# Optimization experiments

Hardware: AMD Instinct MI355X
Metric: run time of the kernel (lower is better)

The kernel has to match this reference:

```python
import jax, jax.numpy as jnp
import numpy as np

N = 50000        # num nodes
E = 800000       # num edges
R = 2            # num relations
HID = 256        # hid_dim
Q = HID // 4     # per-feature-block projection size
NC = 2           # num classes
DES, TW, NP_, CP = 768, 768, 5, 3


def setup_inputs():
    key = jax.random.key(0)
    ks = jax.random.split(key, 32)
    w = lambda i, shape: jax.random.normal(ks[i], shape, dtype=jnp.float32) * 0.05
    z = lambda d: jnp.zeros((d,), jnp.float32)
    return {
        'des': jax.random.normal(ks[0], (N, DES), jnp.float32),
        'tweet': jax.random.normal(ks[1], (N, TW), jnp.float32),
        'num_prop': jax.random.normal(ks[2], (N, NP_), jnp.float32),
        'cat_prop': jax.random.normal(ks[3], (N, CP), jnp.float32),
        'edge_index': jax.random.randint(ks[4], (2, E), 0, N),
        'edge_type': jax.random.randint(ks[5], (E,), 0, R),
        'w_des': w(6, (DES, Q)), 'b_des': z(Q),
        'w_tweet': w(7, (TW, Q)), 'b_tweet': z(Q),
        'w_num': w(8, (NP_, Q)), 'b_num': z(Q),
        'w_cat': w(9, (CP, Q)), 'b_cat': z(Q),
        'w_in': w(10, (HID, HID)), 'b_in': z(HID),
        'weight1': w(11, (R, HID, HID)), 'root1': w(12, (HID, HID)), 'bias1': z(HID),
        'weight2': w(13, (R, HID, HID)), 'root2': w(14, (HID, HID)), 'bias2': z(HID),
        'w_out': w(15, (HID, NC)), 'b_out': z(NC),
    }


def _rgcn_layer(x, weight, root, bias, src, dst, edge_type):
    # T stage: per-relation transform + root transform, bias, relu.
    h_rel = jax.nn.relu(jnp.einsum('nh,rho->rno', x, weight) + bias)   # [R,N,H]
    h_root = jax.nn.relu(x @ root + bias)                              # [N,H]
    # P stage: gather per-relation messages, mean-aggregate at dst, sum over relations.
    msg = h_rel[edge_type, src]                                        # [E,H] gather
    seg = edge_type * N + dst                                          # relation-disjoint segments
    sums = jax.ops.segment_sum(msg, seg, num_segments=R * N).reshape(R, N, -1)
    cnt = jax.ops.segment_sum(jnp.ones((msg.shape[0],), msg.dtype), seg,
                              num_segments=R * N).reshape(R, N, 1)
    mean = sums / jnp.maximum(cnt, 1.0)                                # per-relation mean aggr
    return mean.sum(0) + h_root


def _lrelu(x):
    return jax.nn.leaky_relu(x, 0.01)


def reference(des, tweet, num_prop, cat_prop, edge_index, edge_type,
              w_des, b_des, w_tweet, b_tweet, w_num, b_num, w_cat, b_cat,
              w_in, b_in, weight1, root1, bias1, weight2, root2, bias2,
              w_out, b_out):
    src, dst = edge_index[0], edge_index[1]
    d = _lrelu(des @ w_des + b_des)
    t = _lrelu(tweet @ w_tweet + b_tweet)
    n = _lrelu(num_prop @ w_num + b_num)
    c = _lrelu(cat_prop @ w_cat + b_cat)
    x = jnp.concatenate([d, t, n, c], axis=1)          # [N, HID]
    x = _lrelu(x @ w_in + b_in)
    x = _rgcn_layer(x, weight1, root1, bias1, src, dst, edge_type)
    x = _rgcn_layer(x, weight2, root2, bias2, src, dst, edge_type)
    return x @ w_out + b_out                           # [N, NC] logits (MLP last=True)
```

## Files before the change

kernel.cpp:

```cpp
#include <hip/hip_runtime.h>

#define NN 50000
#define EE 800000
#define HD 256
#define NSEG (2 * NN)
#define CHUNK 2048
#define NB ((NSEG + CHUNK - 1) / CHUNK)

typedef unsigned short u16;
typedef unsigned long long u64;
typedef short bf16x8 __attribute__((ext_vector_type(8)));
typedef float f32x4 __attribute__((ext_vector_type(4)));

__device__ __forceinline__ u16 f2bf_rne(float f) {
    unsigned u = __float_as_uint(f);
    return (u16)((u + 0x7FFF + ((u >> 16) & 1)) >> 16);
}
__device__ __forceinline__ void split_tr(float v, u16& h, u16& l) {
    unsigned u = __float_as_uint(v);
    h = (u16)(u >> 16);
    l = f2bf_rne(v - __uint_as_float(u & 0xFFFF0000u));
}

__device__ __forceinline__ int xcd_swizzle(int orig, int nwg) {
    int q = nwg >> 3, r = nwg & 7;
    int xcd = orig & 7, idx = orig >> 3;
    return (xcd < r ? xcd * (q + 1) : r * (q + 1) + (xcd - r) * q) + idx;
}

__device__ __forceinline__ void g2l16(const void* g, void* l) {
    __builtin_amdgcn_global_load_lds(
        (const __attribute__((address_space(1))) void*)g,
        (__attribute__((address_space(3))) void*)l, 16, 0, 0);
}

__device__ __forceinline__ int swz2(int row) { return (row & 2) | ((row >> 2) & 1); }

__device__ __forceinline__ void stage_bf16(const u16* __restrict__ G, u16* S,
                                           int base_rc, int maxrc, int K, int k0, int tid) {
#pragma unroll
    for (int s = 0; s < 2; s++) {
        int slot = tid + s * 256;
        int row = slot >> 2, gg = slot & 3;
        int gsrc = gg ^ swz2(row);
        int arow = base_rc + row; arow = arow < maxrc ? arow : maxrc - 1;
        g2l16(G + (size_t)arow * K + k0 + gsrc * 8, S + ((tid & ~63) + s * 256) * 8);
    }
}

template<int MODE>
__global__ __launch_bounds__(256) void gemm_bf16s(
    const u16* __restrict__ Ag, const u16* __restrict__ Bg,
    const float* __restrict__ bias,
    u16* __restrict__ O1, float* __restrict__ O2,
    int M, int nxb)
{
    __shared__ __align__(16) u16 sA[2][128 * 32];
    __shared__ __align__(16) u16 sB[2][128 * 32];
    const int wgid = xcd_swizzle(blockIdx.x, gridDim.x);
    const int brow = (wgid / nxb) * 128, bcol = (wgid % nxb) * 128;
    const int tid = threadIdx.x, lane = tid & 63, w = tid >> 6;
    const int wr = w >> 1, wc = w & 1;
    const int r15 = lane & 15, g = lane >> 4;
    const int fsw = (g ^ swz2(r15)) * 8;

    f32x4 acc[4][4];
#pragma unroll
    for (int mi = 0; mi < 4; mi++)
#pragma unroll
        for (int ni = 0; ni < 4; ni++) acc[mi][ni] = (f32x4){0.f, 0.f, 0.f, 0.f};

    auto stage_step = [&](int k0, int b) {
        stage_bf16(Ag, sA[b], brow, M, 256, k0, tid);
        stage_bf16(Bg, sB[b], bcol, 1 << 30, 256, k0, tid);
    };
    auto compute_step = [&](int b) {
        bf16x8 af[4], bf[4];
#pragma unroll
        for (int mi = 0; mi < 4; mi++) {
            int idx = (wr * 64 + mi * 16 + r15) * 32 + fsw;
            af[mi] = *(const bf16x8*)&sA[b][idx];
        }
#pragma unroll
        for (int ni = 0; ni < 4; ni++) {
            int idx = (wc * 64 + ni * 16 + r15) * 32 + fsw;
            bf[ni] = *(const bf16x8*)&sB[b][idx];
        }
#pragma unroll
        for (int mi = 0; mi < 4; mi++)
#pragma unroll
            for (int ni = 0; ni < 4; ni++)
                acc[mi][ni] = __builtin_amdgcn_mfma_f32_16x16x32_bf16(af[mi], bf[ni], acc[mi][ni], 0, 0, 0);
    };

    stage_step(0, 0);
    stage_step(32, 1);
#pragma unroll
    for (int t = 0; t < 7; t++) {
        asm volatile("s_waitcnt vmcnt(4)" ::: "memory");
        __builtin_amdgcn_s_barrier();
        compute_step(t & 1);
        __builtin_amdgcn_s_barrier();
        if (t + 2 < 8) stage_step((t + 2) * 32, t & 1);
    }
    asm volatile("s_waitcnt vmcnt(0)" ::: "memory");
    __builtin_amdgcn_s_barrier();
    compute_step(1);

#pragma unroll
    for (int mi = 0; mi < 4; mi++) {
#pragma unroll
        for (int ni = 0; ni < 4; ni++) {
            int col = bcol + wc * 64 + ni * 16 + r15;
            float bsv = bias[col & (HD - 1)];
            int rbase = brow + wr * 64 + mi * 16 + g * 4;
#pragma unroll
            for (int r = 0; r < 4; r++) {
                int grow = rbase + r;
                if (grow >= M) continue;
                float v = acc[mi][ni][r] + bsv;
                if (MODE == 1) {
                    v = v > 0.f ? v : 0.01f * v;
                    O1[(size_t)grow * HD + col] = f2bf_rne(v);
                } else {
                    v = fmaxf(v, 0.f);
                    if (col < 2 * HD) {
                        O1[((size_t)(col >> 8) * NN + grow) * HD + (col & (HD - 1))] = f2bf_rne(v);
                    } else {
                        O2[(size_t)grow * HD + (col & (HD - 1))] = v;
                    }
                }
            }
        }
    }
}

__global__ __launch_bounds__(128) void gemm_projW(
    const float* __restrict__ A0, const float* __restrict__ A1,
    const u16* __restrict__ B0, const u16* __restrict__ B1,
    const float* __restrict__ bias0, const float* __restrict__ bias1,
    u16* __restrict__ Ch)
{
    __shared__ __align__(16) u16 lds[2 * 2 * 2 * 640];
    const int p = blockIdx.x & 1;
    const float* __restrict__ A = p ? A1 : A0;
    const u16* __restrict__ Bp = p ? B1 : B0;
    const float* __restrict__ bias = p ? bias1 : bias0;
    const int coff = p * 64;
    const int lane = threadIdx.x & 63, w = threadIdx.x >> 6;
    const int wrow = (blockIdx.x >> 1) * 32 + w * 16;
    const int r15 = lane & 15, g = lane >> 4;
    const int lbase = w * 2560;

    size_t aoff[2];
#pragma unroll
    for (int i = 0; i < 2; i++) {
        int row = wrow + (lane >> 3) + 8 * i;
        row = row < NN ? row : NN - 1;
        aoff[i] = (size_t)row * 768 + (lane & 7) * 4;
    }
    size_t boff[4];
#pragma unroll
    for (int ni = 0; ni < 4; ni++)
        boff[ni] = (size_t)(ni * 64 + lane) * 8;

    f32x4 acc[4];
#pragma unroll
    for (int ni = 0; ni < 4; ni++) acc[ni] = (f32x4){0.f, 0.f, 0.f, 0.f};

    float4 Ar0[2], Ar1[2];
    uint4 Bs0[4], Bs1[4];

    auto loadA = [&](int t, float4 (&d)[2]) {
#pragma unroll
        for (int i = 0; i < 2; i++) d[i] = *(const float4*)&A[aoff[i] + t * 32];
    };
    auto loadB = [&](int t, uint4 (&d)[4]) {
#pragma unroll
        for (int ni = 0; ni < 4; ni++) d[ni] = *(const uint4*)&Bp[boff[ni] + (size_t)t * 2048];
    };
    auto writeA = [&](const float4 (&s)[2], int buf) {
#pragma unroll
        for (int i = 0; i < 2; i++) {
            int row2 = (lane >> 3) + 8 * i;
            unsigned e0 = __float_as_uint(s[i].x), e1 = __float_as_uint(s[i].y),
                     e2 = __float_as_uint(s[i].z), e3 = __float_as_uint(s[i].w);
            unsigned h0 = __builtin_amdgcn_perm(e1, e0, 0x07060302u);
            unsigned h1 = __builtin_amdgcn_perm(e3, e2, 0x07060302u);
            unsigned q0 = __float_as_uint(s[i].x - __uint_as_float(e0 & 0xFFFF0000u));
            unsigned q1 = __float_as_uint(s[i].y - __uint_as_float(e1 & 0xFFFF0000u));
            unsigned q2 = __float_as_uint(s[i].z - __uint_as_float(e2 & 0xFFFF0000u));
            unsigned q3 = __float_as_uint(s[i].w - __uint_as_float(e3 & 0xFFFF0000u));
            unsigned l0 = __builtin_amdgcn_perm(q1, q0, 0x07060302u);
            unsigned l1 = __builtin_amdgcn_perm(q3, q2, 0x07060302u);
            int idx = lbase + buf * 1280 + row2 * 40 + (lane & 7) * 4;
            *(u64*)&lds[idx] = (u64)h0 | ((u64)h1 << 32);
            *(u64*)&lds[idx + 640] = (u64)l0 | ((u64)l1 << 32);
        }
    };
    auto compute = [&](int buf, const uint4 (&Bv)[4]) {
        bf16x8 afh, afl;
        {
            int idx = lbase + buf * 1280 + r15 * 40 + g * 8;
            afh = *(const bf16x8*)&lds[idx];
            afl = *(const bf16x8*)&lds[idx + 640];
        }
#pragma unroll
        for (int ni = 0; ni < 4; ni++) {
            bf16x8 bb = __builtin_bit_cast(bf16x8, Bv[ni]);
            acc[ni] = __builtin_amdgcn_mfma_f32_16x16x32_bf16(afh, bb, acc[ni], 0, 0, 0);
            acc[ni] = __builtin_amdgcn_mfma_f32_16x16x32_bf16(afl, bb, acc[ni], 0, 0, 0);
        }
    };

    loadA(0, Ar0); loadB(0, Bs0);
    writeA(Ar0, 0);
    loadA(1, Ar1); loadB(1, Bs1);
    for (int tt = 0; tt < 11; ++tt) {
        int t0 = 2 * tt;
        loadA(t0 + 2, Ar0);
        compute(0, Bs0);
        loadB(t0 + 2, Bs0);
        writeA(Ar1, 1);
        loadA(t0 + 3, Ar1);
        compute(1, Bs1);
        loadB(t0 + 3, Bs1);
        writeA(Ar0, 0);
    }
    compute(0, Bs0);
    writeA(Ar1, 1);
    compute(1, Bs1);

    u16* tlh = &lds[lbase];
#pragma unroll
    for (int ni = 0; ni < 4; ni++) {
        int col = ni * 16 + r15;
        float bsv = bias[col];
#pragma unroll
        for (int r = 0; r < 4; r++) {
            int row = g * 4 + r;
            float v = acc[ni][r] + bsv;
            v = v > 0.f ? v : 0.01f * v;
            tlh[row * 72 + col] = f2bf_rne(v);
        }
    }
    asm volatile("s_waitcnt lgkmcnt(0)" ::: "memory");
    __builtin_amdgcn_sched_barrier(0);
    {
        int row = lane >> 2, cb = (lane & 3) * 16;
        int grow = wrow + row;
        if (grow < NN) {
#pragma unroll
            for (int j = 0; j < 2; j++) {
                uint4 hv = *(const uint4*)&tlh[row * 72 + cb + j * 8];
                *(uint4*)&Ch[(size_t)grow * HD + coff + cb + j * 8] = hv;
            }
        }
    }
}

__global__ void conv_all(
    const float* __restrict__ w_des, const float* __restrict__ w_tw,
    const float* __restrict__ w_in,
    const float* __restrict__ weight1, const float* __restrict__ root1,
    const float* __restrict__ weight2, const float* __restrict__ root2,
    u16* __restrict__ desB, u16* __restrict__ twB,
    u16* __restrict__ winB, u16* __restrict__ cat1, u16* __restrict__ cat2)
{
    const int HSZ = HD * HD;
    int idx = blockIdx.x * 256 + threadIdx.x;
    if (idx < 98304) {
        const float* W = idx < 49152 ? w_des : w_tw;
        u16* Bf = idx < 49152 ? desB : twB;
        int i = idx < 49152 ? idx : idx - 49152;
        int k = i >> 6, n = i & 63;
        int t = k >> 5, kk = k & 31, g = kk >> 3, j = kk & 7;
        int lane = g * 16 + (n & 15), ni = n >> 4;
        Bf[(size_t)((t * 4 + ni) * 64 + lane) * 8 + j] = f2bf_rne(W[i]);
        return;
    }
    int jdx = idx - 98304;
    int seg = jdx >> 16;
    if (seg >= 7) return;
    int i = jdx & 65535;
    const float* srcs[7] = {w_in, weight1, weight1 + HSZ, root1,
                            weight2, weight2 + HSZ, root2};
    u16* dsts[7] = {winB, cat1, cat1 + 256 * 256, cat1 + 512 * 256,
                    cat2, cat2 + 256 * 256, cat2 + 512 * 256};
    int k = i >> 8, n = i & 255;
    dsts[seg][(size_t)n * 256 + k] = f2bf_rne(srcs[seg][i]);
}

__global__ __launch_bounds__(256) void gemm_f32s2(
    const float* __restrict__ A0, const float* __restrict__ A1,
    const float* __restrict__ B0, const float* __restrict__ B1,
    const float* __restrict__ bias0, const float* __restrict__ bias1,
    u16* __restrict__ Ch)
{
    const int p = blockIdx.x;
    const float* __restrict__ A = p ? A1 : A0;
    const float* __restrict__ B = p ? B1 : B0;
    const float* __restrict__ bias = p ? bias1 : bias0;
    const int lda = p ? 3 : 5, K = lda, coff = p ? 192 : 128;

    __shared__ float As[8][64 + 4];
    __shared__ float Bs[8][64 + 4];
    const int tid = threadIdx.x;
    const int tx = tid % 16, ty = tid / 16;
    const int brow = blockIdx.y * 64;
    float acc[4][4];
#pragma unroll
    for (int i = 0; i < 4; i++)
#pragma unroll
        for (int j = 0; j < 4; j++) acc[i][j] = 0.f;

#pragma unroll 2
    for (int idx = tid; idx < 64 * 8; idx += 256) {
        int m = idx / 8, k = idx % 8;
        int gr = brow + m;
        As[k][m] = (gr < NN && k < K) ? A[(size_t)gr * lda + k] : 0.f;
    }
#pragma unroll 2
    for (int idx = tid; idx < 8 * 64; idx += 256) {
        int k = idx / 64, n = idx % 64;
        Bs[k][n] = (k < K) ? B[(size_t)k * 64 + n] : 0.f;
    }
    __syncthreads();
#pragma unroll
    for (int k = 0; k < 8; k++) {
        float a[4], b[4];
#pragma unroll
        for (int i = 0; i < 4; i++) a[i] = As[k][ty * 4 + i];
#pragma unroll
        for (int j = 0; j < 4; j++) b[j] = Bs[k][tx * 4 + j];
#pragma unroll
        for (int i = 0; i < 4; i++)
#pragma unroll
            for (int j = 0; j < 4; j++) acc[i][j] = fmaf(a[i], b[j], acc[i][j]);
    }

#pragma unroll
    for (int i = 0; i < 4; i++) {
        int gr = brow + ty * 4 + i;
        if (gr >= NN) continue;
#pragma unroll
        for (int j = 0; j < 4; j++) {
            int gc = tx * 4 + j;
            float v = acc[i][j] + bias[gc];
            v = v > 0.f ? v : 0.01f * v;
            Ch[(size_t)gr * HD + coff + gc] = f2bf_rne(v);
        }
    }
}

__global__ void count_seg(const int* __restrict__ ei, const int* __restrict__ et,
                          int* __restrict__ segc)
{
    int e = blockIdx.x * blockDim.x + threadIdx.x;
    if (e < EE) {
        int dst = ei[EE + e];
        int r = et[e];
        atomicAdd(&segc[r * NN + dst], 1);
    }
}

__global__ __launch_bounds__(256) void scan_local(const int* __restrict__ segc,
                                                  int* __restrict__ offs,
                                                  int* __restrict__ bsum)
{
    int b = blockIdx.x;
    int base = b * CHUNK;
    int tid = threadIdx.x;
    int lane = tid & 63, wave = tid >> 6;
    __shared__ int wsum[4];
    int vals[8];
    int i0 = base + tid * 8;
    int s = 0;
    if (i0 + 7 < NSEG) {
        int4 v0 = *(const int4*)&segc[i0];
        int4 v1 = *(const int4*)&segc[i0 + 4];
        vals[0] = v0.x; vals[1] = v0.y; vals[2] = v0.z; vals[3] = v0.w;
        vals[4] = v1.x; vals[5] = v1.y; vals[6] = v1.z; vals[7] = v1.w;
    } else {
#pragma unroll
        for (int j = 0; j < 8; j++) vals[j] = (i0 + j < NSEG) ? segc[i0 + j] : 0;
    }
#pragma unroll
    for (int j = 0; j < 8; j++) s += vals[j];
    int v = s;
#pragma unroll
    for (int off = 1; off < 64; off <<= 1) {
        int u = __shfl_up(v, off);
        if (lane >= off) v += u;
    }
    if (lane == 63) wsum[wave] = v;
    __syncthreads();
    int wbase = 0;
#pragma unroll
    for (int ww = 0; ww < 4; ww++) if (ww < wave) wbase += wsum[ww];
    int run = wbase + v - s;
#pragma unroll
    for (int j = 0; j < 8; j++) {
        run += vals[j];
        int i = i0 + j;
        if (i < NSEG) offs[i + 1] = run;
    }
    if (tid == 0) {
        int t = 0;
#pragma unroll
        for (int ww = 0; ww < 4; ww++) t += wsum[ww];
        bsum[b] = t;
    }
}

__global__ void scan_bsum(const int* __restrict__ bsum, int* __restrict__ bbase)
{
    int lane = threadIdx.x;
    int c = (lane < NB) ? bsum[lane] : 0;
    int v = c;
#pragma unroll
    for (int off = 1; off < 64; off <<= 1) {
        int u = __shfl_up(v, off);
        if (lane >= off) v += u;
    }
    if (lane < NB) bbase[lane] = v - c;
}

__global__ void add_base(int* __restrict__ offs, const int* __restrict__ bbase)
{
    int i = blockIdx.x * blockDim.x + threadIdx.x;
    if (i < NSEG) offs[i + 1] += bbase[i / CHUNK];
    if (i == 0) offs[0] = 0;
}

__global__ void fill_src(const int* __restrict__ ei, const int* __restrict__ et,
                         const int* __restrict__ offs, int* __restrict__ cursor,
                         int* __restrict__ src_list)
{
    int e = blockIdx.x * blockDim.x + threadIdx.x;
    if (e < EE) {
        int src = ei[e];
        int dst = ei[EE + e];
        int s = et[e] * NN + dst;
        int pos = offs[s] + atomicAdd(&cursor[s], 1);
        src_list[pos] = src;
    }
}

template<int OUTM>
__global__ __launch_bounds__(256) void gather_mean_b(
    const u16* __restrict__ hrelb,
    const int* __restrict__ offs,
    const int* __restrict__ src_list,
    const float* __restrict__ basein,
    u16* __restrict__ Oh,
    const float* __restrict__ wout, const float* __restrict__ bout,
    float* __restrict__ logits)
{
    int d = blockIdx.x * 4 + (threadIdx.x >> 6);
    if (d >= NN) return;
    int lane = threadIdx.x & 63;
    f32x4 acc = {0.f, 0.f, 0.f, 0.f};
#pragma unroll
    for (int r = 0; r < 2; r++) {
        int s = r * NN + d;
        int start = offs[s], end = offs[s + 1];
        if (start == end) continue;
        f32x4 a = {0.f, 0.f, 0.f, 0.f};
        const u16* hb = hrelb + (size_t)r * NN * HD;
        for (int i = start; i < end; i++) {
            int src = src_list[i];
            uint2 wv = *(const uint2*)(hb + (size_t)src * HD + lane * 4);
            a.x += __uint_as_float(wv.x << 16);
            a.y += __uint_as_float(wv.x & 0xFFFF0000u);
            a.z += __uint_as_float(wv.y << 16);
            a.w += __uint_as_float(wv.y & 0xFFFF0000u);
        }
        float inv = 1.0f / (float)(end - start);
        acc.x += a.x * inv; acc.y += a.y * inv;
        acc.z += a.z * inv; acc.w += a.w * inv;
    }
    float4 b = ((const float4*)(basein + (size_t)d * HD))[lane];
    float v0 = b.x + acc.x, v1 = b.y + acc.y, v2 = b.z + acc.z, v3 = b.w + acc.w;
    if (OUTM == 0) {
        uint2 uh;
        uh.x = (unsigned)f2bf_rne(v0) | ((unsigned)f2bf_rne(v1) << 16);
        uh.y = (unsigned)f2bf_rne(v2) | ((unsigned)f2bf_rne(v3) << 16);
        *(uint2*)(Oh + (size_t)d * HD + lane * 4) = uh;
    } else {
        int k = lane * 4;
        float a0 = v0 * wout[(k + 0) * 2 + 0] + v1 * wout[(k + 1) * 2 + 0]
                 + v2 * wout[(k + 2) * 2 + 0] + v3 * wout[(k + 3) * 2 + 0];
        float a1 = v0 * wout[(k + 0) * 2 + 1] + v1 * wout[(k + 1) * 2 + 1]
                 + v2 * wout[(k + 2) * 2 + 1] + v3 * wout[(k + 3) * 2 + 1];
#pragma unroll
        for (int off = 32; off > 0; off >>= 1) {
            a0 += __shfl_down(a0, off);
            a1 += __shfl_down(a1, off);
        }
        if (lane == 0) {
            logits[(size_t)d * 2 + 0] = a0 + bout[0];
            logits[(size_t)d * 2 + 1] = a1 + bout[1];
        }
    }
}

extern "C" void kernel_launch(void* const* d_in, const int* in_sizes, int n_in,
                              void* d_out, int out_size, void* d_ws, size_t ws_size,
                              hipStream_t stream)
{
    const float* des   = (const float*)d_in[0];
    const float* tweet = (const float*)d_in[1];
    const float* nump  = (const float*)d_in[2];
    const float* catp  = (const float*)d_in[3];
    const int*   ei    = (const int*)d_in[4];
    const int*   et    = (const int*)d_in[5];
    const float* w_des = (const float*)d_in[6],  *b_des = (const float*)d_in[7];
    const float* w_tw  = (const float*)d_in[8],  *b_tw  = (const float*)d_in[9];
    const float* w_num = (const float*)d_in[10], *b_num = (const float*)d_in[11];
    const float* w_cat = (const float*)d_in[12], *b_cat = (const float*)d_in[13];
    const float* w_in  = (const float*)d_in[14], *b_in  = (const float*)d_in[15];
    const float* weight1 = (const float*)d_in[16], *root1 = (const float*)d_in[17], *bias1 = (const float*)d_in[18];
    const float* weight2 = (const float*)d_in[19], *root2 = (const float*)d_in[20], *bias2 = (const float*)d_in[21];
    const float* w_out = (const float*)d_in[22], *b_out = (const float*)d_in[23];
    float* outp = (float*)d_out;

    const int HSZ = HD * HD, PSZ = 768 * 64;

    float* base  = (float*)d_ws;
    u16*   hrelb = (u16*)(base + (size_t)NN * HD);
    u16*   xh    = hrelb + (size_t)2 * NN * HD;
    u16*   yh    = xh + (size_t)NN * HD;
    int*   offs  = (int*)(yh + (size_t)NN * HD);
    int*   segc  = offs + (NSEG + 1);
    int*   srcl  = segc + NSEG;
    int*   bsum  = srcl + EE;
    int*   bbase = bsum + NB;
    uintptr_t wp = ((uintptr_t)(bbase + NB) + 15) & ~(uintptr_t)15;
    u16* desB = (u16*)wp;
    u16* twB  = desB + PSZ;
    u16* winB = twB + PSZ;
    u16* cat1 = winB + HSZ;
    u16* cat2 = cat1 + 3 * HSZ;

    hipMemsetAsync(segc, 0, NSEG * sizeof(int), stream);
    count_seg<<<(EE + 255) / 256, 256, 0, stream>>>(ei, et, segc);
    scan_local<<<NB, 256, 0, stream>>>(segc, offs, bsum);
    scan_bsum<<<1, 64, 0, stream>>>(bsum, bbase);
    add_base<<<(NSEG + 255) / 256, 256, 0, stream>>>(offs, bbase);
    hipMemsetAsync(segc, 0, NSEG * sizeof(int), stream);
    fill_src<<<(EE + 255) / 256, 256, 0, stream>>>(ei, et, offs, segc, srcl);

    const int CONV_TOT = 98304 + 7 * 65536;
    conv_all<<<(CONV_TOT + 255) / 256, 256, 0, stream>>>(
        w_des, w_tw, w_in, weight1, root1, weight2, root2,
        desB, twB, winB, cat1, cat2);

    const int NYB = (NN + 127) / 128;
    const int NWB = (NN + 31) / 32;

    gemm_projW<<<2 * NWB, 128, 0, stream>>>(des, tweet, desB, twB, b_des, b_tw, xh);
    dim3 gsm(2, (NN + 63) / 64);
    gemm_f32s2<<<gsm, 256, 0, stream>>>(nump, catp, w_num, w_cat, b_num, b_cat, xh);

    gemm_bf16s<1><<<2 * NYB, 256, 0, stream>>>(xh, winB, b_in, yh, nullptr, NN, 2);

    gemm_bf16s<2><<<6 * NYB, 256, 0, stream>>>(yh, cat1, bias1, hrelb, base, NN, 6);
    gather_mean_b<0><<<(NN + 3) / 4, 256, 0, stream>>>(hrelb, offs, srcl, base, xh, nullptr, nullptr, nullptr);

    gemm_bf16s<2><<<6 * NYB, 256, 0, stream>>>(xh, cat2, bias2, hrelb, base, NN, 6);
    gather_mean_b<1><<<(NN + 3) / 4, 256, 0, stream>>>(hrelb, offs, srcl, base, nullptr, w_out, b_out, outp);
}
```

Before: 529.6 us.

## Merge independent prologue kernels into heterogeneous mega-launches to cut launch gaps

Independent kernels are combined into heterogeneous launches that branch on block index. The des/tweet projection, small num/cat projection, edge counting and weight conversion now share one launch, and the w_in GEMM shares another with the CSR fill. The fill reuses the count array as a decrementing cursor via atomicSub, which removes the second memset. This is meant to cut launch overhead and let the independent stages overlap on the GPU, at the cost of uneven block shapes within one launch and LDS sized for the largest branch.

```diff
diff --git a/kernel.cpp b/kernel.cpp
--- a/kernel.cpp
+++ b/kernel.cpp
@@ -16,11 +16,6 @@
     unsigned u = __float_as_uint(f);
     return (u16)((u + 0x7FFF + ((u >> 16) & 1)) >> 16);
 }
-__device__ __forceinline__ void split_tr(float v, u16& h, u16& l) {
-    unsigned u = __float_as_uint(v);
-    h = (u16)(u >> 16);
-    l = f2bf_rne(v - __uint_as_float(u & 0xFFFF0000u));
-}
 
 __device__ __forceinline__ int xcd_swizzle(int orig, int nwg) {
     int q = nwg >> 3, r = nwg & 7;
@@ -49,15 +44,15 @@
 }
 
 template<int MODE>
-__global__ __launch_bounds__(256) void gemm_bf16s(
+__device__ __forceinline__ void gemm_body(
+    u16* __restrict__ sA, u16* __restrict__ sB,
+    int bid, int nwg,
     const u16* __restrict__ Ag, const u16* __restrict__ Bg,
     const float* __restrict__ bias,
     u16* __restrict__ O1, float* __restrict__ O2,
     int M, int nxb)
 {
-    __shared__ __align__(16) u16 sA[2][128 * 32];
-    __shared__ __align__(16) u16 sB[2][128 * 32];
-    const int wgid = xcd_swizzle(blockIdx.x, gridDim.x);
+    const int wgid = xcd_swizzle(bid, nwg);
     const int brow = (wgid / nxb) * 128, bcol = (wgid % nxb) * 128;
     const int tid = threadIdx.x, lane = tid & 63, w = tid >> 6;
     const int wr = w >> 1, wc = w & 1;
@@ -71,20 +66,20 @@
         for (int ni = 0; ni < 4; ni++) acc[mi][ni] = (f32x4){0.f, 0.f, 0.f, 0.f};
 
     auto stage_step = [&](int k0, int b) {
-        stage_bf16(Ag, sA[b], brow, M, 256, k0, tid);
-        stage_bf16(Bg, sB[b], bcol, 1 << 30, 256, k0, tid);
+        stage_bf16(Ag, sA + b * 4096, brow, M, 256, k0, tid);
+        stage_bf16(Bg, sB + b * 4096, bcol, 1 << 30, 256, k0, tid);
     };
     auto compute_step = [&](int b) {
         bf16x8 af[4], bf[4];
 #pragma unroll
         for (int mi = 0; mi < 4; mi++) {
             int idx = (wr * 64 + mi * 16 + r15) * 32 + fsw;
-            af[mi] = *(const bf16x8*)&sA[b][idx];
+            af[mi] = *(const bf16x8*)&sA[b * 4096 + idx];
         }
 #pragma unroll
         for (int ni = 0; ni < 4; ni++) {
             int idx = (wc * 64 + ni * 16 + r15) * 32 + fsw;
-            bf[ni] = *(const bf16x8*)&sB[b][idx];
+            bf[ni] = *(const bf16x8*)&sB[b * 4096 + idx];
         }
 #pragma unroll
         for (int mi = 0; mi < 4; mi++)
@@ -135,20 +130,32 @@
     }
 }
 
-__global__ __launch_bounds__(128) void gemm_projW(
+template<int MODE>
+__global__ __launch_bounds__(256) void gemm_bf16s(
+    const u16* __restrict__ Ag, const u16* __restrict__ Bg,
+    const float* __restrict__ bias,
+    u16* __restrict__ O1, float* __restrict__ O2,
+    int M, int nxb)
+{
+    __shared__ __align__(16) u16 sA[2 * 4096];
+    __shared__ __align__(16) u16 sB[2 * 4096];
+    gemm_body<MODE>(sA, sB, blockIdx.x, gridDim.x, Ag, Bg, bias, O1, O2, M, nxb);
+}
+
+__device__ __forceinline__ void projW_body(
+    u16* __restrict__ lds, int bid,
     const float* __restrict__ A0, const float* __restrict__ A1,
     const u16* __restrict__ B0, const u16* __restrict__ B1,
     const float* __restrict__ bias0, const float* __restrict__ bias1,
     u16* __restrict__ Ch)
 {
-    __shared__ __align__(16) u16 lds[2 * 2 * 2 * 640];
-    const int p = blockIdx.x & 1;
+    const int p = bid & 1;
     const float* __restrict__ A = p ? A1 : A0;
     const u16* __restrict__ Bp = p ? B1 : B0;
     const float* __restrict__ bias = p ? bias1 : bias0;
     const int coff = p * 64;
     const int lane = threadIdx.x & 63, w = threadIdx.x >> 6;
-    const int wrow = (blockIdx.x >> 1) * 32 + w * 16;
+    const int wrow = (bid >> 1) * 32 + w * 16;
     const int r15 = lane & 15, g = lane >> 4;
     const int lbase = w * 2560;
 
@@ -259,86 +266,57 @@
     }
 }
 
-__global__ void conv_all(
-    const float* __restrict__ w_des, const float* __restrict__ w_tw,
-    const float* __restrict__ w_in,
-    const float* __restrict__ weight1, const float* __restrict__ root1,
-    const float* __restrict__ weight2, const float* __restrict__ root2,
-    u16* __restrict__ desB, u16* __restrict__ twB,
-    u16* __restrict__ winB, u16* __restrict__ cat1, u16* __restrict__ cat2)
-{
-    const int HSZ = HD * HD;
-    int idx = blockIdx.x * 256 + threadIdx.x;
-    if (idx < 98304) {
-        const float* W = idx < 49152 ? w_des : w_tw;
-        u16* Bf = idx < 49152 ? desB : twB;
-        int i = idx < 49152 ? idx : idx - 49152;
-        int k = i >> 6, n = i & 63;
-        int t = k >> 5, kk = k & 31, g = kk >> 3, j = kk & 7;
-        int lane = g * 16 + (n & 15), ni = n >> 4;
-        Bf[(size_t)((t * 4 + ni) * 64 + lane) * 8 + j] = f2bf_rne(W[i]);
-        return;
-    }
-    int jdx = idx - 98304;
-    int seg = jdx >> 16;
-    if (seg >= 7) return;
-    int i = jdx & 65535;
-    const float* srcs[7] = {w_in, weight1, weight1 + HSZ, root1,
-                            weight2, weight2 + HSZ, root2};
-    u16* dsts[7] = {winB, cat1, cat1 + 256 * 256, cat1 + 512 * 256,
-                    cat2, cat2 + 256 * 256, cat2 + 512 * 256};
-    int k = i >> 8, n = i & 255;
-    dsts[seg][(size_t)n * 256 + k] = f2bf_rne(srcs[seg][i]);
-}
-
-__global__ __launch_bounds__(256) void gemm_f32s2(
-    const float* __restrict__ A0, const float* __restrict__ A1,
-    const float* __restrict__ B0, const float* __restrict__ B1,
-    const float* __restrict__ bias0, const float* __restrict__ bias1,
+__device__ __forceinline__ void smallproj_body(
+    float* __restrict__ smem, int sbid,
+    const float* __restrict__ nump, const float* __restrict__ catp,
+    const float* __restrict__ w_num, const float* __restrict__ w_cat,
+    const float* __restrict__ b_num, const float* __restrict__ b_cat,
     u16* __restrict__ Ch)
 {
-    const int p = blockIdx.x;
-    const float* __restrict__ A = p ? A1 : A0;
-    const float* __restrict__ B = p ? B1 : B0;
-    const float* __restrict__ bias = p ? bias1 : bias0;
-    const int lda = p ? 3 : 5, K = lda, coff = p ? 192 : 128;
-
-    __shared__ float As[8][64 + 4];
-    __shared__ float Bs[8][64 + 4];
+    const int NSB = (NN + 31) / 32;
+    const int p = sbid >= NSB;
+    const int brow = (p ? sbid - NSB : sbid) * 32;
+    const float* __restrict__ A = p ? catp : nump;
+    const float* __restrict__ B = p ? w_cat : w_num;
+    const float* __restrict__ bias = p ? b_cat : b_num;
+    const int K = p ? 3 : 5, coff = p ? 192 : 128;
     const int tid = threadIdx.x;
-    const int tx = tid % 16, ty = tid / 16;
-    const int brow = blockIdx.y * 64;
+    float* As = smem;
+    float* Bs = smem + 8 * 36;
+
+#pragma unroll
+    for (int s = 0; s < 2; s++) {
+        int idx = tid + s * 128;
+        int m = idx >> 3, k = idx & 7;
+        int gr = brow + m;
+        As[k * 36 + m] = (gr < NN && k < K) ? A[(size_t)gr * K + k] : 0.f;
+    }
+#pragma unroll
+    for (int s = 0; s < 4; s++) {
+        int idx = tid + s * 128;
+        int k = idx >> 6, n = idx & 63;
+        Bs[k * 68 + n] = (k < K) ? B[k * 64 + n] : 0.f;
+    }
+    __syncthreads();
+
+    const int tx = tid & 15, ty = tid >> 4;
     float acc[4][4];
 #pragma unroll
     for (int i = 0; i < 4; i++)
 #pragma unroll
         for (int j = 0; j < 4; j++) acc[i][j] = 0.f;
-
-#pragma unroll 2
-    for (int idx = tid; idx < 64 * 8; idx += 256) {
-        int m = idx / 8, k = idx % 8;
-        int gr = brow + m;
-        As[k][m] = (gr < NN && k < K) ? A[(size_t)gr * lda + k] : 0.f;
-    }
-#pragma unroll 2
-    for (int idx = tid; idx < 8 * 64; idx += 256) {
-        int k = idx / 64, n = idx % 64;
-        Bs[k][n] = (k < K) ? B[(size_t)k * 64 + n] : 0.f;
-    }
-    __syncthreads();
 #pragma unroll
     for (int k = 0; k < 8; k++) {
         float a[4], b[4];
 #pragma unroll
-        for (int i = 0; i < 4; i++) a[i] = As[k][ty * 4 + i];
-#pragma unroll
-        for (int j = 0; j < 4; j++) b[j] = Bs[k][tx * 4 + j];
+        for (int i = 0; i < 4; i++) a[i] = As[k * 36 + ty * 4 + i];
+#pragma unroll
+        for (int j = 0; j < 4; j++) b[j] = Bs[k * 68 + tx * 4 + j];
 #pragma unroll
         for (int i = 0; i < 4; i++)
 #pragma unroll
             for (int j = 0; j < 4; j++) acc[i][j] = fmaf(a[i], b[j], acc[i][j]);
     }
-
 #pragma unroll
     for (int i = 0; i < 4; i++) {
         int gr = brow + ty * 4 + i;
@@ -353,15 +331,95 @@
     }
 }
 
-__global__ void count_seg(const int* __restrict__ ei, const int* __restrict__ et,
-                          int* __restrict__ segc)
-{
-    int e = blockIdx.x * blockDim.x + threadIdx.x;
+__global__ __launch_bounds__(128) void mega1(
+    const float* __restrict__ des, const float* __restrict__ tweet,
+    const u16* __restrict__ desB, const u16* __restrict__ twB,
+    const float* __restrict__ b_des, const float* __restrict__ b_tw,
+    u16* __restrict__ xh,
+    const float* __restrict__ nump, const float* __restrict__ catp,
+    const float* __restrict__ w_num, const float* __restrict__ w_cat,
+    const float* __restrict__ b_num, const float* __restrict__ b_cat,
+    const int* __restrict__ ei, const int* __restrict__ et, int* __restrict__ segc,
+    const float* __restrict__ w_in,
+    const float* __restrict__ weight1, const float* __restrict__ root1,
+    const float* __restrict__ weight2, const float* __restrict__ root2,
+    u16* __restrict__ winB, u16* __restrict__ cat1, u16* __restrict__ cat2,
+    int nproj, int nsmall, int ncount)
+{
+    __shared__ __align__(16) u16 smem[5120];
+    int bid = blockIdx.x;
+    if (bid < nproj) {
+        projW_body(smem, bid, des, tweet, desB, twB, b_des, b_tw, xh);
+        return;
+    }
+    bid -= nproj;
+    if (bid < nsmall) {
+        smallproj_body((float*)smem, bid, nump, catp, w_num, w_cat, b_num, b_cat, xh);
+        return;
+    }
+    bid -= nsmall;
+    if (bid < ncount) {
+        int e = bid * 128 + threadIdx.x;
+        if (e < EE) {
+            int dst = ei[EE + e];
+            int r = et[e];
+            atomicAdd(&segc[r * NN + dst], 1);
+        }
+        return;
+    }
+    bid -= ncount;
+    {
+        const int HSZ = HD * HD;
+        int idx = bid * 128 + threadIdx.x;
+        int seg = idx >> 16;
+        if (seg >= 7) return;
+        int i = idx & 65535;
+        const float* srcs[7] = {w_in, weight1, weight1 + HSZ, root1,
+                                weight2, weight2 + HSZ, root2};
+        u16* dsts[7] = {winB, cat1, cat1 + 256 * 256, cat1 + 512 * 256,
+                        cat2, cat2 + 256 * 256, cat2 + 512 * 256};
+        int k = i >> 8, n = i & 255;
+        dsts[seg][(size_t)n * 256 + k] = f2bf_rne(srcs[seg][i]);
+    }
+}
+
+__global__ __launch_bounds__(256) void mega2(
+    const u16* __restrict__ xh, const u16* __restrict__ winB,
+    const float* __restrict__ b_in, u16* __restrict__ yh,
+    const int* __restrict__ ei, const int* __restrict__ et,
+    const int* __restrict__ offs, int* __restrict__ cursor,
+    int* __restrict__ src_list,
+    int nwin)
+{
+    __shared__ __align__(16) u16 sA[2 * 4096];
+    __shared__ __align__(16) u16 sB[2 * 4096];
+    int bid = blockIdx.x;
+    if (bid < nwin) {
+        gemm_body<1>(sA, sB, bid, nwin, xh, winB, b_in, yh, nullptr, NN, 2);
+        return;
+    }
+    int e = (bid - nwin) * 256 + threadIdx.x;
     if (e < EE) {
+        int src = ei[e];
         int dst = ei[EE + e];
-        int r = et[e];
-        atomicAdd(&segc[r * NN + dst], 1);
-    }
+        int s = et[e] * NN + dst;
+        int old = atomicSub(&cursor[s], 1);
+        src_list[offs[s] + old - 1] = src;
+    }
+}
+
+__global__ void conv_proj(const float* __restrict__ w_des, const float* __restrict__ w_tw,
+                          u16* __restrict__ desB, u16* __restrict__ twB)
+{
+    int idx = blockIdx.x * 256 + threadIdx.x;
+    if (idx >= 98304) return;
+    const float* W = idx < 49152 ? w_des : w_tw;
+    u16* Bf = idx < 49152 ? desB : twB;
+    int i = idx < 49152 ? idx : idx - 49152;
+    int k = i >> 6, n = i & 63;
+    int t = k >> 5, kk = k & 31, g = kk >> 3, j = kk & 7;
+    int lane = g * 16 + (n & 15), ni = n >> 4;
+    Bf[(size_t)((t * 4 + ni) * 64 + lane) * 8 + j] = f2bf_rne(W[i]);
 }
 
 __global__ __launch_bounds__(256) void scan_local(const int* __restrict__ segc,
@@ -431,20 +489,6 @@
     int i = blockIdx.x * blockDim.x + threadIdx.x;
     if (i < NSEG) offs[i + 1] += bbase[i / CHUNK];
     if (i == 0) offs[0] = 0;
-}
-
-__global__ void fill_src(const int* __restrict__ ei, const int* __restrict__ et,
-                         const int* __restrict__ offs, int* __restrict__ cursor,
-                         int* __restrict__ src_list)
-{
-    int e = blockIdx.x * blockDim.x + threadIdx.x;
-    if (e < EE) {
-        int src = ei[e];
-        int dst = ei[EE + e];
-        int s = et[e] * NN + dst;
-        int pos = offs[s] + atomicAdd(&cursor[s], 1);
-        src_list[pos] = src;
-    }
 }
 
 template<int OUTM>
@@ -543,31 +587,32 @@
     u16* cat1 = winB + HSZ;
     u16* cat2 = cat1 + 3 * HSZ;
 
+    const int NYB = (NN + 127) / 128;
+    const int NWB = (NN + 31) / 32;
+    const int NSB = (NN + 31) / 32;
+
     hipMemsetAsync(segc, 0, NSEG * sizeof(int), stream);
-    count_seg<<<(EE + 255) / 256, 256, 0, stream>>>(ei, et, segc);
+    conv_proj<<<(98304 + 255) / 256, 256, 0, stream>>>(w_des, w_tw, desB, twB);
+    const int nproj = 2 * NWB;
+    const int nsmall = 2 * NSB;
+    const int ncount = (EE + 127) / 128;
+    const int nconv = (7 * 65536 + 127) / 128;
+    mega1<<<nproj + nsmall + ncount + nconv, 128, 0, stream>>>(
+        des, tweet, desB, twB, b_des, b_tw, xh,
+        nump, catp, w_num, w_cat, b_num, b_cat,
+        ei, et, segc,
+        w_in, weight1, root1, weight2, root2,
+        winB, cat1, cat2,
+        nproj, nsmall, ncount);
     scan_local<<<NB, 256, 0, stream>>>(segc, offs, bsum);
     scan_bsum<<<1, 64, 0, stream>>>(bsum, bbase);
     add_base<<<(NSEG + 255) / 256, 256, 0, stream>>>(offs, bbase);
-    hipMemsetAsync(segc, 0, NSEG * sizeof(int), stream);
-    fill_src<<<(EE + 255) / 256, 256, 0, stream>>>(ei, et, offs, segc, srcl);
-
-    const int CONV_TOT = 98304 + 7 * 65536;
-    conv_all<<<(CONV_TOT + 255) / 256, 256, 0, stream>>>(
-        w_des, w_tw, w_in, weight1, root1, weight2, root2,
-        desB, twB, winB, cat1, cat2);
-
-    const int NYB = (NN + 127) / 128;
-    const int NWB = (NN + 31) / 32;
-
-    gemm_projW<<<2 * NWB, 128, 0, stream>>>(des, tweet, desB, twB, b_des, b_tw, xh);
-    dim3 gsm(2, (NN + 63) / 64);
-    gemm_f32s2<<<gsm, 256, 0, stream>>>(nump, catp, w_num, w_cat, b_num, b_cat, xh);
-
-    gemm_bf16s<1><<<2 * NYB, 256, 0, stream>>>(xh, winB, b_in, yh, nullptr, NN, 2);
-
+    const int nwin = 2 * NYB;
+    const int nfill = (EE + 255) / 256;
+    mega2<<<nwin + nfill, 256, 0, stream>>>(xh, winB, b_in, yh,
+                                            ei, et, offs, segc, srcl, nwin);
     gemm_bf16s<2><<<6 * NYB, 256, 0, stream>>>(yh, cat1, bias1, hrelb, base, NN, 6);
     gather_mean_b<0><<<(NN + 3) / 4, 256, 0, stream>>>(hrelb, offs, srcl, base, xh, nullptr, nullptr, nullptr);
-
     gemm_bf16s<2><<<6 * NYB, 256, 0, stream>>>(xh, cat2, bias2, hrelb, base, NN, 6);
     gather_mean_b<1><<<(NN + 3) / 4, 256, 0, stream>>>(hrelb, offs, srcl, base, nullptr, w_out, b_out, outp);
 }
```

Result: faster. 486.3 us (-8.2%).
